# Performance work log

Hardware: AMD Instinct MI355X
Metric: run time of the kernel (lower is better)

Reference implementation:

```python
import jax, jax.numpy as jnp
import numpy as np

N_LAYER, N_HEAD, N_EMBD, VOCAB, T_CTX, MAXT, B = 6, 8, 128, 18, 30, 2719, 64


def _ln(x, g, b, eps=1e-5):
    m = x.mean(-1, keepdims=True)
    v = ((x - m) ** 2).mean(-1, keepdims=True)
    return (x - m) * jax.lax.rsqrt(v + eps) * g + b


def setup_inputs() -> dict:
    key = jax.random.key(0)
    ks = iter(jax.random.split(key, 64))
    nrm = lambda shape: jax.random.normal(next(ks), shape, jnp.float32) * 0.02
    E, L4 = N_EMBD, 4 * N_EMBD
    inp = dict(
        states=jax.random.normal(next(ks), (B, T_CTX, 4, 84, 84), jnp.float32),
        actions=jax.random.randint(next(ks), (B, T_CTX, 1), 0, VOCAB),
        rtgs=jax.random.normal(next(ks), (B, T_CTX, 1), jnp.float32),
        timesteps=jax.random.randint(next(ks), (B, 1, 1), 0, MAXT),
        conv_w=nrm((E, 4, 84, 84)),
        class_tok=nrm((1, 1, E)),
        in_proj_w=nrm((3 * E, E)), in_proj_b=jnp.zeros(3 * E),
        out_w=nrm((E, E)), out_b=jnp.zeros(E),
        iln1_g=jnp.ones(E), iln1_b=jnp.zeros(E),
        iln2_g=jnp.ones(E), iln2_b=jnp.zeros(E),
        ffn_w1=nrm((E, E)), ffn_b1=jnp.zeros(E),
        ffn_w2=nrm((E, E)), ffn_b2=jnp.zeros(E),
        ret_w=nrm((E, 1)), ret_b=jnp.zeros(E),
        act_table=nrm((VOCAB, E)),
        pos_emb=nrm((1, 3 * T_CTX + 1, E)),
        global_pos_emb=nrm((1, MAXT + 1, E)),
        ln1_g=jnp.ones((N_LAYER, E)), ln1_b=jnp.zeros((N_LAYER, E)),
        Wq=nrm((N_LAYER, E, E)), bq=jnp.zeros((N_LAYER, E)),
        Wk=nrm((N_LAYER, E, E)), bk=jnp.zeros((N_LAYER, E)),
        Wv=nrm((N_LAYER, E, E)), bv=jnp.zeros((N_LAYER, E)),
        Wo=nrm((N_LAYER, E, E)), bo=jnp.zeros((N_LAYER, E)),
        ln2_g=jnp.ones((N_LAYER, E)), ln2_b=jnp.zeros((N_LAYER, E)),
        W1=nrm((N_LAYER, L4, E)), b1=jnp.zeros((N_LAYER, L4)),
        W2=nrm((N_LAYER, E, L4)), b2=jnp.zeros((N_LAYER, E)),
        lnf_g=jnp.ones(E), lnf_b=jnp.zeros(E),
        head_w=nrm((VOCAB, E)),
    )
    return inp


def _forward(states, actions, rtgs, timesteps, conv_w, class_tok, in_proj_w, in_proj_b,
             out_w, out_b, iln1_g, iln1_b, iln2_g, iln2_b, ffn_w1, ffn_b1, ffn_w2, ffn_b2,
             ret_w, ret_b, act_table, pos_emb, global_pos_emb,
             ln1_g, ln1_b, Wq, bq, Wk, bk, Wv, bv, Wo, bo, ln2_g, ln2_b,
             W1, b1, W2, b2, lnf_g, lnf_b, head_w):
    Bsz, T = states.shape[:2]
    E = conv_w.shape[0]
    H, hd = N_HEAD, E // N_HEAD
    # --- inner TIT: patch embed (kernel 84 = frame size -> single patch = one big dot) ---
    obs = states.reshape(Bsz * T, *states.shape[2:])                      # (BT,4,84,84)
    patch = jnp.einsum('bchw,echw->be', obs, conv_w)[:, None, :]          # (BT,1,E)
    x = jnp.concatenate([jnp.broadcast_to(class_tok, (Bsz * T, 1, E)), patch], axis=1)  # (BT,2,E)
    h = _ln(x, iln1_g, iln1_b)
    q, k, v = jnp.split(h @ in_proj_w.T + in_proj_b, 3, axis=-1)
    att = jax.nn.softmax(jnp.einsum('bqe,bke->bqk', q, k) / jnp.sqrt(jnp.float32(E)), axis=-1)
    x = x + jnp.einsum('bqk,bke->bqe', att, v) @ out_w.T + out_b
    h2 = _ln(x, iln2_g, iln2_b)
    x = x + jax.nn.relu(h2 @ ffn_w1.T + ffn_b1) @ ffn_w2.T + ffn_b2
    state_emb = x[:, 0, :].reshape(Bsz, T, E)                             # class token
    # --- token interleave (targets=None path -> length 3T-1, last T-1 actions) ---
    rtg_emb = jnp.tanh(rtgs @ ret_w.T + ret_b)                            # (B,T,E)
    act_emb = jnp.tanh(act_table[actions[..., 0]])                        # (B,T,E)
    Lt = 3 * T - 1
    tok = jnp.zeros((Bsz, Lt, E), states.dtype)
    tok = tok.at[:, 0::3].set(rtg_emb).at[:, 1::3].set(state_emb).at[:, 2::3].set(act_emb[:, 1:])
    pos = global_pos_emb[0][timesteps[:, 0, 0]][:, None, :] + pos_emb[:, :Lt, :]
    x = tok + pos
    # --- outer causal GPT blocks ---
    mask = jnp.tril(jnp.ones((Lt, Lt), bool))
    for i in range(N_LAYER):
        hh = _ln(x, ln1_g[i], ln1_b[i])
        proj = lambda w, b: (hh @ w.T + b).reshape(Bsz, Lt, H, hd).transpose(0, 2, 1, 3)
        q, k, v = proj(Wq[i], bq[i]), proj(Wk[i], bk[i]), proj(Wv[i], bv[i])
        att = jnp.einsum('bhqd,bhkd->bhqk', q, k) / jnp.sqrt(jnp.float32(hd))
        att = jax.nn.softmax(jnp.where(mask, att, -jnp.inf), axis=-1)
        y = jnp.einsum('bhqk,bhkd->bhqd', att, v).transpose(0, 2, 1, 3).reshape(Bsz, Lt, E)
        x = x + y @ Wo[i].T + bo[i]
        hh2 = _ln(x, ln2_g[i], ln2_b[i])
        x = x + jax.nn.gelu(hh2 @ W1[i].T + b1[i], approximate=False) @ W2[i].T + b2[i]
    logits = _ln(x, lnf_g, lnf_b) @ head_w.T
    return logits[:, 1::3, :]                                             # (B,T,vocab) state-position logits


def reference(states, actions, rtgs, timesteps, conv_w, class_tok, in_proj_w, in_proj_b,
              out_w, out_b, iln1_g, iln1_b, iln2_g, iln2_b, ffn_w1, ffn_b1, ffn_w2, ffn_b2,
              ret_w, ret_b, act_table, pos_emb, global_pos_emb,
              ln1_g, ln1_b, Wq, bq, Wk, bk, Wv, bv, Wo, bo, ln2_g, ln2_b,
              W1, b1, W2, b2, lnf_g, lnf_b, head_w):
    return _forward(states, actions, rtgs, timesteps, conv_w, class_tok, in_proj_w, in_proj_b,
                    out_w, out_b, iln1_g, iln1_b, iln2_g, iln2_b, ffn_w1, ffn_b1, ffn_w2, ffn_b2,
                    ret_w, ret_b, act_table, pos_emb, global_pos_emb,
                    ln1_g, ln1_b, Wq, bq, Wk, bk, Wv, bv, Wo, bo, ln2_g, ln2_b,
                    W1, b1, W2, b2, lnf_g, lnf_b, head_w)
```

## Files before the change

kernel.cpp:

```cpp
#include <hip/hip_runtime.h>

#define NB   64
#define NT   30
#define NBT  1920
#define EE   128
#define KP   28224
#define LTK  89
#define NS   5696
#define NLY  6
#define NV   18
#define NZ   21

typedef unsigned short ushort_t;
using bf16x8 = __attribute__((ext_vector_type(8))) short;
using us8    = __attribute__((ext_vector_type(8))) unsigned short;
using f32x4  = __attribute__((ext_vector_type(4))) float;
using f32x16 = __attribute__((ext_vector_type(16))) float;

__device__ inline ushort_t f2bf(float f){
  union { float f; unsigned u; } v; v.f = f;
  unsigned r = v.u + 0x7FFFu + ((v.u >> 16) & 1u);
  return (ushort_t)(r >> 16);
}

__global__ __launch_bounds__(256) void wcvt(
  const float* conv, const float* Wq, const float* Wk, const float* Wv,
  const float* Wo, const float* W1, const float* W2,
  const float* in_w, const float* out_w, const float* f1w, const float* f2w,
  const float* bq, const float* bk, const float* bv,
  ushort_t* dc, ushort_t* dqkv, ushort_t* dout, ushort_t* d1, ushort_t* d2,
  ushort_t* dinw, ushort_t* doutw, ushort_t* df1, ushort_t* df2, float* bqkv)
{
  if (blockIdx.x >= 4776){
    int idx = (blockIdx.x-4776)*256 + threadIdx.x;
    if (idx < NLY*128){ int l=idx>>7, j=idx&127;
      bqkv[l*384+j]=bq[idx]; bqkv[l*384+128+j]=bk[idx]; bqkv[l*384+256+j]=bv[idx]; }
    return;
  }
  long i = 4l*((long)blockIdx.x*256 + threadIdx.x);
  if (i >= 3612672l && i < 3907584l){
    long o = i - 3612672l;
    int  seg = (int)(o / 98304l);
    long off2 = o - (long)seg*98304l;
    long layer = off2 >> 14, rem = off2 & 16383l;
    const float* s = (seg==0) ? Wq : (seg==1) ? Wk : Wv;
    float4 f = *reinterpret_cast<const float4*>(s+off2);
    long dst = layer*49152l + (long)seg*16384l + rem;
    dqkv[dst]=f2bf(f.x); dqkv[dst+1]=f2bf(f.y); dqkv[dst+2]=f2bf(f.z); dqkv[dst+3]=f2bf(f.w);
    return;
  }
  const float* s; ushort_t* d; long off;
  if      (i < 3612672l){ s=conv;  d=dc;    off=i; }
  else if (i < 4005888l){ s=Wo;    d=dout;  off=i-3907584l; }
  else if (i < 4399104l){ s=W1;    d=d1;    off=i-4005888l; }
  else if (i < 4792320l){ s=W2;    d=d2;    off=i-4399104l; }
  else if (i < 4841472l){ s=in_w;  d=dinw;  off=i-4792320l; }
  else if (i < 4857856l){ s=out_w; d=doutw; off=i-4841472l; }
  else if (i < 4874240l){ s=f1w;   d=df1;   off=i-4857856l; }
  else                  { s=f2w;   d=df2;   off=i-4874240l; }
  float4 f = *reinterpret_cast<const float4*>(s+off);
  d[off]=f2bf(f.x); d[off+1]=f2bf(f.y); d[off+2]=f2bf(f.z); d[off+3]=f2bf(f.w);
}

__global__ __launch_bounds__(256) void patch_gemm(
  const float* __restrict__ A, const ushort_t* __restrict__ Wb, float* __restrict__ C)
{
  __shared__ __align__(16) ushort_t As[2][64*64];
  __shared__ __align__(16) ushort_t Ws[2][128*64];
  const int tid = threadIdx.x, lane = tid & 63, wid = tid >> 6;
  const int m0 = blockIdx.x * 64;
  const int kbase = blockIdx.z * 1344;
  float* Cz = C + (size_t)blockIdx.z * NBT * EE;
  const int ra = tid>>2, ca = (tid&3)*16, swa = (ra&7)<<3;
  const int rw = tid>>1, cw = (tid&1)*32, sww = (rw&7)<<3;
  const float*    Ab = A  + (size_t)(m0+ra)*KP + kbase + ca;
  const ushort_t* Wp = Wb + (size_t)rw*KP  + kbase + cw;
  f32x4 acc[8];
  #pragma unroll
  for (int j=0;j<8;j++) acc[j] = (f32x4){0.f,0.f,0.f,0.f};

  auto loadT = [&](float4 (&fa)[4], us8 (&wr)[4], int kt){
    #pragma unroll
    for (int q=0;q<4;q++){
      fa[q] = *reinterpret_cast<const float4*>(Ab + kt*64 + 4*q);
      wr[q] = *reinterpret_cast<const us8*>(Wp + kt*64 + 8*q);
    }
  };
  auto commitT = [&](int buf, const float4 (&fa)[4], const us8 (&wr)[4]){
    us8 o0, o1;
    o0[0]=f2bf(fa[0].x); o0[1]=f2bf(fa[0].y); o0[2]=f2bf(fa[0].z); o0[3]=f2bf(fa[0].w);
    o0[4]=f2bf(fa[1].x); o0[5]=f2bf(fa[1].y); o0[6]=f2bf(fa[1].z); o0[7]=f2bf(fa[1].w);
    o1[0]=f2bf(fa[2].x); o1[1]=f2bf(fa[2].y); o1[2]=f2bf(fa[2].z); o1[3]=f2bf(fa[2].w);
    o1[4]=f2bf(fa[3].x); o1[5]=f2bf(fa[3].y); o1[6]=f2bf(fa[3].z); o1[7]=f2bf(fa[3].w);
    *reinterpret_cast<us8*>(&As[buf][ra*64 + ( ca    ^ swa)]) = o0;
    *reinterpret_cast<us8*>(&As[buf][ra*64 + ((ca+8) ^ swa)]) = o1;
    #pragma unroll
    for (int q=0;q<4;q++)
      *reinterpret_cast<us8*>(&Ws[buf][rw*64 + ((cw+8*q) ^ sww)]) = wr[q];
  };
  auto computeT = [&](int buf){
    #pragma unroll
    for (int ks=0; ks<2; ++ks){
      int arow = wid*16 + (lane&15);
      int kb = ks*32 + (lane>>4)*8;
      bf16x8 a = *reinterpret_cast<const bf16x8*>(&As[buf][arow*64 + (kb ^ ((arow&7)<<3))]);
      #pragma unroll
      for (int nt=0; nt<8; ++nt){
        int nn = nt*16 + (lane&15);
        bf16x8 b = *reinterpret_cast<const bf16x8*>(&Ws[buf][nn*64 + (kb ^ ((nn&7)<<3))]);
        acc[nt] = __builtin_amdgcn_mfma_f32_16x16x32_bf16(a, b, acc[nt], 0,0,0);
      }
    }
  };

  float4 faA[4], faB[4]; us8 wrA[4], wrB[4];
  loadT(faA, wrA, 0);
  loadT(faB, wrB, 1);
  for (int kp = 0; kp < 11; ++kp){
    int kt0 = 2*kp;
    commitT(0, faA, wrA);
    if (kt0 + 2 < 21) loadT(faA, wrA, kt0 + 2);
    __syncthreads();
    computeT(0);
    int kt1 = kt0 + 1;
    if (kt1 < 21){
      commitT(1, faB, wrB);
      if (kt1 + 2 < 21) loadT(faB, wrB, kt1 + 2);
      __syncthreads();
      computeT(1);
    }
  }
  #pragma unroll
  for (int nt=0; nt<8; ++nt)
    #pragma unroll
    for (int rr=0;rr<4;rr++){
      int row = m0 + wid*16 + (lane>>4)*4 + rr;
      int col = nt*16 + (lane&15);
      Cz[row*EE + col] = acc[nt][rr];
    }
}

__global__ __launch_bounds__(256, 1) void inner_tit(
  const float* __restrict__ part, const float* __restrict__ ctok,
  const ushort_t* __restrict__ inw, const float* __restrict__ in_b,
  const ushort_t* __restrict__ outw, const float* __restrict__ out_b,
  const float* __restrict__ g1, const float* __restrict__ b1_,
  const float* __restrict__ g2, const float* __restrict__ b2_,
  const ushort_t* __restrict__ f1wb, const float* __restrict__ fb1,
  const ushort_t* __restrict__ f2wb, const float* __restrict__ fb2,
  const float* __restrict__ rtgs, const int* __restrict__ actions,
  const int* __restrict__ tsteps, const float* __restrict__ ret_w,
  const float* __restrict__ ret_b, const float* __restrict__ act_tab,
  const float* __restrict__ pos_emb, const float* __restrict__ gpos,
  const float* __restrict__ ln1g0, const float* __restrict__ ln1b0,
  float* __restrict__ x, ushort_t* __restrict__ xln)
{
  __shared__ __align__(16) ushort_t wbuf[384*128];
  __shared__ float xs[16*128];
  __shared__ __align__(16) ushort_t hb[16*128];
  __shared__ __align__(16) ushort_t hf[16*128];
  __shared__ float qkv[16*384];
  __shared__ float ssm[32];
  const int tid = threadIdx.x, lane = tid & 63, wid = tid >> 6;
  const int bt0 = blockIdx.x * 8;

  auto stageWB = [&](const ushort_t* src, int R, int rowoff){
    for (int c = tid; c < R*16; c += 256){
      int rr = c >> 4, cc = (c & 15) * 8;
      *reinterpret_cast<us8*>(&wbuf[(rowoff+rr)*128 + (cc ^ ((rr&7)<<3))]) =
        *reinterpret_cast<const us8*>(src + (size_t)rr*128 + cc);
    }
  };
  auto lnrow = [&](const float* gam, const float* bet, ushort_t* dst){
    int r = tid >> 4, e0 = (tid & 15) * 8;
    float v[8];
    #pragma unroll
    for (int j=0;j<8;j++) v[j] = xs[r*128 + e0 + j];
    float s = 0;
    #pragma unroll
    for (int j=0;j<8;j++) s += v[j];
    s += __shfl_xor(s,1); s += __shfl_xor(s,2); s += __shfl_xor(s,4); s += __shfl_xor(s,8);
    float mean = s * (1.0f/128.0f);
    float vs = 0;
    #pragma unroll
    for (int j=0;j<8;j++){ float d = v[j]-mean; vs += d*d; }
    vs += __shfl_xor(vs,1); vs += __shfl_xor(vs,2); vs += __shfl_xor(vs,4); vs += __shfl_xor(vs,8);
    float rstd = rsqrtf(vs*(1.0f/128.0f) + 1e-5f);
    us8 o;
    #pragma unroll
    for (int j=0;j<8;j++) o[j] = f2bf((v[j]-mean)*rstd*gam[e0+j] + bet[e0+j]);
    *reinterpret_cast<us8*>(&dst[r*128 + (e0 ^ ((r&7)<<3))]) = o;
  };

  { int r = tid >> 4, e0 = (tid & 15) * 8;
    float v[8];
    if ((r & 1) == 0){
      #pragma unroll
      for (int j=0;j<8;j++) v[j] = ctok[e0+j];
    } else {
      #pragma unroll
      for (int j=0;j<8;j++) v[j] = 0.f;
      int bt = bt0 + (r>>1);
      for (int z=0; z<NZ; ++z){
        const float* p = part + (size_t)z*NBT*EE + (size_t)bt*128 + e0;
        float4 f0 = *reinterpret_cast<const float4*>(p);
        float4 f1 = *reinterpret_cast<const float4*>(p+4);
        v[0]+=f0.x; v[1]+=f0.y; v[2]+=f0.z; v[3]+=f0.w;
        v[4]+=f1.x; v[5]+=f1.y; v[6]+=f1.z; v[7]+=f1.w;
      }
    }
    #pragma unroll
    for (int j=0;j<8;j++) xs[r*128 + e0 + j] = v[j];
  }
  stageWB(inw, 384, 0);
  __syncthreads();

  lnrow(g1, b1_, hb);
  __syncthreads();

  { int al = lane & 15, kq = (lane>>4)*8;
    #pragma unroll
    for (int j=0;j<6;++j){
      int nt = wid*6 + j;
      f32x4 acc = (f32x4){0.f,0.f,0.f,0.f};
      int nrow = nt*16 + al, nsw = (nrow&7)<<3;
      #pragma unroll
      for (int ks=0; ks<4; ++ks){
        int kb = ks*32 + kq;
        bf16x8 a = *reinterpret_cast<const bf16x8*>(&hb[al*128 + (kb ^ ((al&7)<<3))]);
        bf16x8 b = *reinterpret_cast<const bf16x8*>(&wbuf[nrow*128 + (kb ^ nsw)]);
        acc = __builtin_amdgcn_mfma_f32_16x16x32_bf16(a, b, acc, 0,0,0);
      }
      float bia = in_b[nt*16 + al];
      #pragma unroll
      for (int rr=0; rr<4; ++rr){
        int row = (lane>>4)*4 + rr;
        qkv[row*384 + nt*16 + al] = acc[rr] + bia;
      }
    }
  }
  __syncthreads();

  { int d = tid >> 3, j = tid & 7;
    int i = d >> 2, p = d & 3;
    const float* qp = &qkv[(2*i + (p>>1))*384 + j*16];
    const float* kp = &qkv[(2*i + (p&1))*384 + 128 + j*16];
    float s = 0;
    #pragma unroll
    for (int e=0;e<16;e++) s += qp[e]*kp[e];
    s += __shfl_xor(s,1); s += __shfl_xor(s,2); s += __shfl_xor(s,4);
    if (j == 0) ssm[d] = s;
  }
  stageWB(outw, 128, 0);
  stageWB(f1wb, 128, 128);
  stageWB(f2wb, 128, 256);
  __syncthreads();

  { int r = tid >> 4, e0 = (tid & 15)*8;
    int i = r >> 1, t = r & 1;
    const float sc = 0.08838834764831845f;
    float s0 = ssm[i*4 + t*2]*sc, s1 = ssm[i*4 + t*2 + 1]*sc;
    float m = fmaxf(s0,s1), p0 = __expf(s0-m), p1 = __expf(s1-m);
    float iv = 1.0f/(p0+p1); p0 *= iv; p1 *= iv;
    const float* v0 = &qkv[(2*i)*384 + 256 + e0];
    const float* v1 = &qkv[(2*i+1)*384 + 256 + e0];
    us8 o;
    #pragma unroll
    for (int j=0;j<8;j++) o[j] = f2bf(p0*v0[j] + p1*v1[j]);
    *reinterpret_cast<us8*>(&hb[r*128 + (e0 ^ ((r&7)<<3))]) = o;
  }
  __syncthreads();

  { int al = lane & 15, kq = (lane>>4)*8;
    #pragma unroll
    for (int j=0;j<2;++j){
      int nt = wid*2 + j;
      f32x4 acc = (f32x4){0.f,0.f,0.f,0.f};
      int nrow = nt*16 + al, nsw = (nrow&7)<<3;
      #pragma unroll
      for (int ks=0; ks<4; ++ks){
        int kb = ks*32 + kq;
        bf16x8 a = *reinterpret_cast<const bf16x8*>(&hb[al*128 + (kb ^ ((al&7)<<3))]);
        bf16x8 b = *reinterpret_cast<const bf16x8*>(&wbuf[nrow*128 + (kb ^ nsw)]);
        acc = __builtin_amdgcn_mfma_f32_16x16x32_bf16(a, b, acc, 0,0,0);
      }
      float bia = out_b[nt*16 + al];
      #pragma unroll
      for (int rr=0; rr<4; ++rr){
        int row = (lane>>4)*4 + rr;
        xs[row*128 + nt*16 + al] += acc[rr] + bia;
      }
    }
  }
  __syncthreads();

  lnrow(g2, b2_, hb);
  __syncthreads();

  { int al = lane & 15, kq = (lane>>4)*8;
    #pragma unroll
    for (int j=0;j<2;++j){
      int nt = wid*2 + j;
      f32x4 acc = (f32x4){0.f,0.f,0.f,0.f};
      int nrow = nt*16 + al, nsw = (nrow&7)<<3;
      #pragma unroll
      for (int ks=0; ks<4; ++ks){
        int kb = ks*32 + kq;
        bf16x8 a = *reinterpret_cast<const bf16x8*>(&hb[al*128 + (kb ^ ((al&7)<<3))]);
        bf16x8 b = *reinterpret_cast<const bf16x8*>(&wbuf[(128+nrow)*128 + (kb ^ nsw)]);
        acc = __builtin_amdgcn_mfma_f32_16x16x32_bf16(a, b, acc, 0,0,0);
      }
      float bia = fb1[nt*16 + al];
      #pragma unroll
      for (int rr=0; rr<4; ++rr){
        int row = (lane>>4)*4 + rr;
        hf[row*128 + ((nt*16+al) ^ ((row&7)<<3))] = f2bf(fmaxf(acc[rr] + bia, 0.f));
      }
    }
  }
  __syncthreads();

  { int al = lane & 15, kq = (lane>>4)*8;
    #pragma unroll
    for (int j=0;j<2;++j){
      int nt = wid*2 + j;
      f32x4 acc = (f32x4){0.f,0.f,0.f,0.f};
      int nrow = nt*16 + al, nsw = (nrow&7)<<3;
      #pragma unroll
      for (int ks=0; ks<4; ++ks){
        int kb = ks*32 + kq;
        bf16x8 a = *reinterpret_cast<const bf16x8*>(&hf[al*128 + (kb ^ ((al&7)<<3))]);
        bf16x8 b = *reinterpret_cast<const bf16x8*>(&wbuf[(256+nrow)*128 + (kb ^ nsw)]);
        acc = __builtin_amdgcn_mfma_f32_16x16x32_bf16(a, b, acc, 0,0,0);
      }
      float bia = fb2[nt*16 + al];
      #pragma unroll
      for (int rr=0; rr<4; ++rr){
        int row = (lane>>4)*4 + rr;
        xs[row*128 + nt*16 + al] += acc[rr] + bia;
      }
    }
  }
  __syncthreads();

  { int q = tid >> 3, j = tid & 7;
    if (q < 24){
      int i = q / 3, kind = q - 3*i;
      int btg = bt0 + i, b = btg / NT, t = btg - b*NT;
      bool valid = !(kind == 2 && t == 0);
      if (valid){
        int prow = (kind==0) ? 3*t : (kind==1) ? 3*t+1 : 3*t-1;
        size_t xrow = ((size_t)b*LTK + prow)*128;
        int ts = tsteps[b];
        int e0 = j*16;
        float v[16];
        if (kind == 1){
          #pragma unroll
          for (int e=0;e<16;e++) v[e] = xs[(2*i)*128 + e0 + e];
        } else if (kind == 0){
          float rv = rtgs[b*NT+t];
          #pragma unroll
          for (int e=0;e<16;e++) v[e] = tanhf(rv*ret_w[e0+e] + ret_b[e0+e]);
        } else {
          int a = actions[b*NT+t];
          #pragma unroll
          for (int e=0;e<16;e++) v[e] = tanhf(act_tab[a*128 + e0 + e]);
        }
        #pragma unroll
        for (int e=0;e<16;e++)
          v[e] += gpos[(size_t)ts*128 + e0 + e] + pos_emb[prow*128 + e0 + e];
        #pragma unroll
        for (int e=0;e<16;e++) x[xrow + e0 + e] = v[e];
        float s = 0;
        #pragma unroll
        for (int e=0;e<16;e++) s += v[e];
        s += __shfl_xor(s,1); s += __shfl_xor(s,2); s += __shfl_xor(s,4);
        float mean = s * (1.0f/128.0f);
        float vs = 0;
        #pragma unroll
        for (int e=0;e<16;e++){ float d = v[e]-mean; vs += d*d; }
        vs += __shfl_xor(vs,1); vs += __shfl_xor(vs,2); vs += __shfl_xor(vs,4);
        float rstd = rsqrtf(vs*(1.0f/128.0f) + 1e-5f);
        #pragma unroll
        for (int e=0;e<16;e++)
          xln[xrow + e0 + e] = f2bf((v[e]-mean)*rstd*ln1g0[e0+e] + ln1b0[e0+e]);
      }
    }
  }
}

__global__ __launch_bounds__(256, 2) void attn_fused(
  const ushort_t* __restrict__ xln, const ushort_t* __restrict__ Wqkv,
  const float* __restrict__ bqkv, ushort_t* __restrict__ y)
{
  __shared__ __align__(16) char sm[69504];
  ushort_t* ab  = (ushort_t*)sm;
  ushort_t* wb  = (ushort_t*)(sm + 24576);
  float*    S   = (float*)sm;
  ushort_t* qa  = (ushort_t*)(sm + 37248);
  ushort_t* ka  = (ushort_t*)(sm + 41472);
  ushort_t* vta = (ushort_t*)(sm + 45696);
  ushort_t* pb  = (ushort_t*)(sm + 49152);
  float*    inv = (float*)(sm + 69120);

  const int b = blockIdx.x >> 3, h = blockIdx.x & 7;
  const int tid = threadIdx.x, lane = tid & 63, wid = tid >> 6;

  for (int idx = tid; idx < 1536; idx += 256){
    int row = idx >> 4, c0 = (idx & 15) * 8;
    us8 v;
    if (row < LTK) v = *reinterpret_cast<const us8*>(xln + ((size_t)(b*LTK+row))*128 + c0);
    else           v = (us8){0,0,0,0,0,0,0,0};
    *reinterpret_cast<us8*>(&ab[row*128 + (c0 ^ ((row&7)<<3))]) = v;
  }
  for (int idx = tid; idx < 384; idx += 256){
    int rr = idx >> 3, c = (idx & 7) * 16;
    int seg = rr >> 4, n = rr & 15;
    const ushort_t* src = Wqkv + (size_t)(seg*128 + h*16 + n)*128 + c;
    int sw = (rr&7)<<3;
    *reinterpret_cast<us8*>(&wb[rr*128 + ( c    ^ sw)]) = *reinterpret_cast<const us8*>(src);
    *reinterpret_cast<us8*>(&wb[rr*128 + ((c+8) ^ sw)]) = *reinterpret_cast<const us8*>(src+8);
  }
  __syncthreads();

  for (int idx = wid; idx < 18; idx += 4){
    int rt = idx / 3, nt = idx - 3*(idx/3);
    f32x4 acc = (f32x4){0.f,0.f,0.f,0.f};
    int arow = rt*16 + (lane&15), asw = (arow&7)<<3;
    int nrow = nt*16 + (lane&15), nsw = (nrow&7)<<3;
    #pragma unroll
    for (int ks=0; ks<4; ++ks){
      int kb = ks*32 + (lane>>4)*8;
      bf16x8 a = *reinterpret_cast<const bf16x8*>(&ab[arow*128 + (kb ^ asw)]);
      bf16x8 bf = *reinterpret_cast<const bf16x8*>(&wb[nrow*128 + (kb ^ nsw)]);
      acc = __builtin_amdgcn_mfma_f32_16x16x32_bf16(a, bf, acc, 0,0,0);
    }
    int d = lane & 15;
    float bia = bqkv[nt*128 + h*16 + d];
    #pragma unroll
    for (int rr=0; rr<4; ++rr){
      int rg = rt*16 + (lane>>4)*4 + rr;
      ushort_t hv = f2bf(acc[rr] + bia);
      if      (nt == 0) qa[rg*22 + d] = hv;
      else if (nt == 1) ka[rg*22 + d] = hv;
      else              vta[d*108 + rg] = hv;
    }
  }
  __syncthreads();

  {
    static const int TR[6] = {0,1,1,2,2,2};
    static const int TC[6] = {0,0,1,0,1,2};
    for (int idx = wid; idx < 6; idx += 4){
      int R = TR[idx], C = TC[idx];
      int arow = R*32 + (lane&31), brow = C*32 + (lane&31);
      int ke = (lane>>5)*8;
      bf16x8 a  = *reinterpret_cast<const bf16x8*>(&qa[arow*22 + ke]);
      bf16x8 bf = *reinterpret_cast<const bf16x8*>(&ka[brow*22 + ke]);
      f32x16 sc = {};
      sc = __builtin_amdgcn_mfma_f32_32x32x16_bf16(a, bf, sc, 0,0,0);
      #pragma unroll
      for (int r=0; r<16; ++r){
        int rin = (r&3) + 8*(r>>2) + 4*(lane>>5);
        S[(R*32+rin)*97 + C*32 + (lane&31)] = sc[r]*0.25f;
      }
    }
  }
  __syncthreads();

  if (tid < 192){
    int t = tid >> 1, half = tid & 1;
    int u0 = half*48;
    float mx = -1e30f;
    if (t < LTK){
      for (int u=u0; u<u0+48; ++u) if (u<=t) mx = fmaxf(mx, S[t*97+u]);
    }
    mx = fmaxf(mx, __shfl_xor(mx,1));
    float smv = 0;
    if (t < LTK){
      for (int u=u0; u<u0+48; ++u){
        float p = 0;
        if (u<=t){ p = __expf(S[t*97+u]-mx); smv += p; }
        pb[t*104+u] = f2bf(p);
      }
    } else {
      for (int u=u0; u<u0+48; ++u) pb[t*104+u] = 0;
    }
    smv += __shfl_xor(smv,1);
    if (half==0) inv[t] = (t<LTK) ? 1.0f/smv : 0.0f;
  }
  __syncthreads();

  for (int rt = wid; rt < 6; rt += 4){
    int arow = rt*16 + (lane&15);
    f32x4 acc = (f32x4){0.f,0.f,0.f,0.f};
    #pragma unroll
    for (int ks=0; ks<3; ++ks){
      int kb = ks*32 + (lane>>4)*8;
      bf16x8 a  = *reinterpret_cast<const bf16x8*>(&pb[arow*104 + kb]);
      bf16x8 bf = *reinterpret_cast<const bf16x8*>(&vta[(lane&15)*108 + kb]);
      acc = __builtin_amdgcn_mfma_f32_16x16x32_bf16(a, bf, acc, 0,0,0);
    }
    #pragma unroll
    for (int rr=0; rr<4; ++rr){
      int rg = rt*16 + (lane>>4)*4 + rr;
      if (rg < LTK)
        y[(size_t)(b*LTK+rg)*128 + h*16 + (lane&15)] = f2bf(acc[rr]*inv[rg]);
    }
  }
}

template<bool HEAD>
__global__ __launch_bounds__(256, 2) void ffn_fused(
  const ushort_t* __restrict__ yg, const ushort_t* __restrict__ Wo,
  const float* __restrict__ bo, const float* __restrict__ g2,
  const float* __restrict__ b2g, const ushort_t* __restrict__ W1,
  const float* __restrict__ b1v, const ushort_t* __restrict__ W2,
  const float* __restrict__ b2v, float* __restrict__ x,
  const float* __restrict__ lnng, const float* __restrict__ lnnb,
  ushort_t* __restrict__ xlnout,
  const float* __restrict__ lnfg, const float* __restrict__ lnfb,
  const float* __restrict__ hw, float* __restrict__ out)
{
  __shared__ __align__(16) char sm[66304];
  ushort_t* wdb = (ushort_t*)sm;
  float*    xr  = (float*)(sm + 32768);
  ushort_t* h2  = (ushort_t*)(sm + 49664);
  ushort_t* f1  = (ushort_t*)(sm + 57856);
  const int tid = threadIdx.x, lane = tid & 63, wid = tid >> 6;
  const int m0 = blockIdx.x * 32;
  const int rr = tid >> 2, qq = tid & 3, swr = (rr&7)<<3;

  auto srcp = [&](int s)->const ushort_t* {
    if (s == 0) return Wo + (size_t)rr*128 + qq*32;
    if (s == 1) return Wo + (size_t)(64+rr)*128 + qq*32;
    int c = (s-2)>>2, r = (s-2)&3;
    if (r == 0) return W1 + (size_t)(c*128+rr)*128 + qq*32;
    if (r == 1) return W1 + (size_t)(c*128+64+rr)*128 + qq*32;
    if (r == 2) return W2 + (size_t)rr*512 + c*128 + qq*32;
    return W2 + (size_t)(64+rr)*512 + c*128 + qq*32;
  };
  auto issue = [&](us8 (&r)[4], int s){
    const ushort_t* p = srcp(s);
    #pragma unroll
    for (int g=0; g<4; ++g) r[g] = *reinterpret_cast<const us8*>(p + 8*g);
  };
  auto commit = [&](int buf, const us8 (&r)[4]){
    ushort_t* d = wdb + buf*8192 + rr*128;
    #pragma unroll
    for (int g=0; g<4; ++g)
      *reinterpret_cast<us8*>(&d[(qq*32+8*g) ^ swr]) = r[g];
  };
  auto gemmT = [&](const ushort_t* abuf, int buf, f32x4* accp){
    int nrow = wid*16 + (lane&15), nsw = (nrow&7)<<3;
    const ushort_t* wbp = wdb + buf*8192;
    #pragma unroll
    for (int rt=0; rt<2; ++rt){
      int arow = rt*16 + (lane&15), asw = (arow&7)<<3;
      #pragma unroll
      for (int ks=0; ks<4; ++ks){
        int kb = ks*32 + (lane>>4)*8;
        bf16x8 a  = *reinterpret_cast<const bf16x8*>(&abuf[arow*128 + (kb ^ asw)]);
        bf16x8 bb = *reinterpret_cast<const bf16x8*>(&wdb[buf*8192 + nrow*128 + (kb ^ nsw)]);
        accp[rt] = __builtin_amdgcn_mfma_f32_16x16x32_bf16(a, bb, accp[rt], 0,0,0);
      }
    }
    (void)wbp;
  };

  f32x4 accA[2][2], acc2[2][2];
  #pragma unroll
  for (int s_=0;s_<2;++s_){
    accA[s_][0]=(f32x4){0,0,0,0}; accA[s_][1]=(f32x4){0,0,0,0};
    acc2[s_][0]=(f32x4){0,0,0,0}; acc2[s_][1]=(f32x4){0,0,0,0};
  }

  auto computeStage = [&](int k, int buf){
    if (k == 0){
      gemmT(f1, buf, accA[0]);
    } else if (k == 1){
      gemmT(f1, buf, accA[1]);
      #pragma unroll
      for (int s_=0; s_<2; ++s_){
        int col = s_*64 + wid*16 + (lane&15);
        float bia = bo[col];
        #pragma unroll
        for (int rt=0; rt<2; ++rt)
          #pragma unroll
          for (int r4=0; r4<4; ++r4){
            int row = rt*16 + (lane>>4)*4 + r4;
            xr[row*132 + col] = accA[s_][rt][r4] + bia + x[(size_t)(m0+row)*128 + col];
          }
      }
      __syncthreads();
      { int r8 = tid>>3, q8 = tid&7;
        float xv[16];
        #pragma unroll
        for (int i=0;i<16;i++) xv[i] = xr[r8*132 + q8*16 + i];
        float s = 0;
        #pragma unroll
        for (int i=0;i<16;i++) s += xv[i];
        s += __shfl_xor(s,1); s += __shfl_xor(s,2); s += __shfl_xor(s,4);
        float mean = s * (1.0f/128.0f);
        float vs = 0;
        #pragma unroll
        for (int i=0;i<16;i++){ float d = xv[i]-mean; vs += d*d; }
        vs += __shfl_xor(vs,1); vs += __shfl_xor(vs,2); vs += __shfl_xor(vs,4);
        float rstd = rsqrtf(vs*(1.0f/128.0f) + 1e-5f);
        int sw = (r8&7)<<3;
        #pragma unroll
        for (int g=0; g<2; ++g){
          us8 o;
          #pragma unroll
          for (int jj=0;jj<8;jj++){
            int c = q8*16 + g*8 + jj;
            o[jj] = f2bf((xv[g*8+jj]-mean)*rstd*g2[c] + b2g[c]);
          }
          *reinterpret_cast<us8*>(&h2[r8*128 + ((q8*16+g*8) ^ sw)]) = o;
        }
      }
    } else {
      int r = (k-2)&3, c = (k-2)>>2;
      if (r < 2){
        f32x4 ac[2] = {(f32x4){0,0,0,0},(f32x4){0,0,0,0}};
        gemmT(h2, buf, ac);
        int cl = r*64 + wid*16 + (lane&15);
        float bia = b1v[c*128 + cl];
        #pragma unroll
        for (int rt=0; rt<2; ++rt)
          #pragma unroll
          for (int r4=0; r4<4; ++r4){
            int row = rt*16 + (lane>>4)*4 + r4;
            float v = ac[rt][r4] + bia;
            v = 0.5f*v*(1.0f + erff(v*0.70710678118654752f));
            f1[row*128 + (cl ^ ((row&7)<<3))] = f2bf(v);
          }
      } else if (r == 2){
        gemmT(f1, buf, acc2[0]);
      } else {
        gemmT(f1, buf, acc2[1]);
      }
    }
  };

  { int r8 = tid>>3, q8 = tid&7, sw = (r8&7)<<3;
    const ushort_t* src = yg + (size_t)(m0+r8)*128 + q8*16;
    *reinterpret_cast<us8*>(&f1[r8*128 + ((q8*16)   ^ sw)]) = *reinterpret_cast<const us8*>(src);
    *reinterpret_cast<us8*>(&f1[r8*128 + ((q8*16+8) ^ sw)]) = *reinterpret_cast<const us8*>(src+8);
  }
  us8 rA[4], rB[4];
  issue(rA, 0); issue(rB, 1);

  for (int kp = 0; kp < 9; ++kp){
    int k0 = 2*kp, k1 = 2*kp + 1;
    commit(0, rA);
    if (k0 + 2 < 18) issue(rA, k0 + 2);
    __syncthreads();
    computeStage(k0, 0);
    commit(1, rB);
    if (k1 + 2 < 18) issue(rB, k1 + 2);
    __syncthreads();
    computeStage(k1, 1);
  }

  #pragma unroll
  for (int s_=0; s_<2; ++s_){
    int col = s_*64 + wid*16 + (lane&15);
    float bia = b2v[col];
    #pragma unroll
    for (int rt=0; rt<2; ++rt)
      #pragma unroll
      for (int r4=0; r4<4; ++r4){
        int row = rt*16 + (lane>>4)*4 + r4;
        float v = acc2[s_][rt][r4] + bia + xr[row*132 + col];
        xr[row*132 + col] = v;
        if constexpr (!HEAD) x[(size_t)(m0+row)*128 + col] = v;
      }
  }
  __syncthreads();
  if constexpr (!HEAD){
    int r8 = tid>>3, q8 = tid&7;
    float xv[16];
    #pragma unroll
    for (int i=0;i<16;i++) xv[i] = xr[r8*132 + q8*16 + i];
    float s = 0;
    #pragma unroll
    for (int i=0;i<16;i++) s += xv[i];
    s += __shfl_xor(s,1); s += __shfl_xor(s,2); s += __shfl_xor(s,4);
    float mean = s * (1.0f/128.0f);
    float vs = 0;
    #pragma unroll
    for (int i=0;i<16;i++){ float d = xv[i]-mean; vs += d*d; }
    vs += __shfl_xor(vs,1); vs += __shfl_xor(vs,2); vs += __shfl_xor(vs,4);
    float rstd = rsqrtf(vs*(1.0f/128.0f) + 1e-5f);
    #pragma unroll
    for (int g=0; g<2; ++g){
      us8 o;
      #pragma unroll
      for (int jj=0;jj<8;jj++){
        int c = q8*16 + g*8 + jj;
        o[jj] = f2bf((xv[g*8+jj]-mean)*rstd*lnng[c] + lnnb[c]);
      }
      *reinterpret_cast<us8*>(xlnout + (size_t)(m0+r8)*128 + q8*16 + g*8) = o;
    }
  } else {
    for (int r = wid; r < 32; r += 4){
      int s = m0 + r, bb2 = s / LTK, p = s - bb2*LTK;
      if (p % 3 != 1) continue;
      int t = p / 3;
      float v1 = xr[r*132 + lane];
      float v2 = xr[r*132 + 64 + lane];
      float sum = v1 + v2;
      sum += __shfl_xor(sum,1); sum += __shfl_xor(sum,2); sum += __shfl_xor(sum,4);
      sum += __shfl_xor(sum,8); sum += __shfl_xor(sum,16); sum += __shfl_xor(sum,32);
      float mean = sum*(1.0f/128.0f);
      float d1 = v1-mean, d2 = v2-mean;
      float var = d1*d1 + d2*d2;
      var += __shfl_xor(var,1); var += __shfl_xor(var,2); var += __shfl_xor(var,4);
      var += __shfl_xor(var,8); var += __shfl_xor(var,16); var += __shfl_xor(var,32);
      float rstd = rsqrtf(var*(1.0f/128.0f) + 1e-5f);
      float h1 = d1*rstd*lnfg[lane]    + lnfb[lane];
      float h2v= d2*rstd*lnfg[lane+64] + lnfb[lane+64];
      #pragma unroll
      for (int o=0; o<NV; ++o){
        float sdot = h1*hw[o*128+lane] + h2v*hw[o*128+lane+64];
        sdot += __shfl_xor(sdot,1); sdot += __shfl_xor(sdot,2); sdot += __shfl_xor(sdot,4);
        sdot += __shfl_xor(sdot,8); sdot += __shfl_xor(sdot,16); sdot += __shfl_xor(sdot,32);
        if (lane == 0) out[(size_t)(bb2*NT+t)*NV + o] = sdot;
      }
    }
  }
}

extern "C" void kernel_launch(void* const* d_in, const int* in_sizes, int n_in,
                              void* d_out, int out_size, void* d_ws, size_t ws_size,
                              hipStream_t stream)
{
  const float* states  = (const float*)d_in[0];
  const int*   actions = (const int*)  d_in[1];
  const float* rtgs    = (const float*)d_in[2];
  const int*   tsteps  = (const int*)  d_in[3];
  const float* conv_w  = (const float*)d_in[4];
  const float* ctok    = (const float*)d_in[5];
  const float* in_w    = (const float*)d_in[6];
  const float* in_b    = (const float*)d_in[7];
  const float* out_w   = (const float*)d_in[8];
  const float* out_b   = (const float*)d_in[9];
  const float* i1g     = (const float*)d_in[10];
  const float* i1b     = (const float*)d_in[11];
  const float* i2g     = (const float*)d_in[12];
  const float* i2b     = (const float*)d_in[13];
  const float* fw1     = (const float*)d_in[14];
  const float* fb1     = (const float*)d_in[15];
  const float* fw2     = (const float*)d_in[16];
  const float* fb2     = (const float*)d_in[17];
  const float* ret_w   = (const float*)d_in[18];
  const float* ret_b   = (const float*)d_in[19];
  const float* act_tab = (const float*)d_in[20];
  const float* pos_emb = (const float*)d_in[21];
  const float* gpos    = (const float*)d_in[22];
  const float* ln1g    = (const float*)d_in[23];
  const float* ln1b    = (const float*)d_in[24];
  const float* Wq      = (const float*)d_in[25];
  const float* bq      = (const float*)d_in[26];
  const float* Wk      = (const float*)d_in[27];
  const float* bk      = (const float*)d_in[28];
  const float* Wv      = (const float*)d_in[29];
  const float* bv      = (const float*)d_in[30];
  const float* Wo      = (const float*)d_in[31];
  const float* bo      = (const float*)d_in[32];
  const float* ln2g    = (const float*)d_in[33];
  const float* ln2b    = (const float*)d_in[34];
  const float* W1      = (const float*)d_in[35];
  const float* b1      = (const float*)d_in[36];
  const float* W2      = (const float*)d_in[37];
  const float* b2      = (const float*)d_in[38];
  const float* lnfg    = (const float*)d_in[39];
  const float* lnfb    = (const float*)d_in[40];
  const float* head_w  = (const float*)d_in[41];

  char* w = (char*)d_ws;
  size_t off = 0;
  auto alloc = [&](size_t bytes)->char* {
    char* p = w + off; off += (bytes + 255) & ~(size_t)255; return p;
  };
  float*    part  = (float*)   alloc((size_t)NZ*NBT*EE*4);
  float*    x     = (float*)   alloc((size_t)NS*EE*4);
  ushort_t* xlnA  = (ushort_t*)alloc((size_t)NS*EE*2);
  ushort_t* xlnB  = (ushort_t*)alloc((size_t)NS*EE*2);
  ushort_t* yb    = (ushort_t*)alloc((size_t)NS*EE*2);
  ushort_t* cwb   = (ushort_t*)alloc((size_t)EE*KP*2);
  ushort_t* Wqkvb = (ushort_t*)alloc((size_t)NLY*384*128*2);
  ushort_t* Wob   = (ushort_t*)alloc((size_t)NLY*128*128*2);
  ushort_t* W1b   = (ushort_t*)alloc((size_t)NLY*512*128*2);
  ushort_t* W2b   = (ushort_t*)alloc((size_t)NLY*128*512*2);
  ushort_t* inwb  = (ushort_t*)alloc((size_t)384*128*2);
  ushort_t* outwb = (ushort_t*)alloc((size_t)128*128*2);
  ushort_t* f1wb  = (ushort_t*)alloc((size_t)128*128*2);
  ushort_t* f2wb  = (ushort_t*)alloc((size_t)128*128*2);
  float*    bqkv  = (float*)   alloc(NLY*384*4);
  (void)in_sizes; (void)n_in; (void)out_size; (void)ws_size;

  wcvt<<<4779,256,0,stream>>>(conv_w,Wq,Wk,Wv,Wo,W1,W2,
                              in_w,out_w,fw1,fw2, bq,bk,bv,
                              cwb,Wqkvb,Wob,W1b,W2b,
                              inwb,outwb,f1wb,f2wb, bqkv);
  patch_gemm<<<dim3(30,1,NZ),256,0,stream>>>(states, cwb, part);
  inner_tit<<<240,256,0,stream>>>(part, ctok, inwb, in_b, outwb, out_b,
                                  i1g,i1b,i2g,i2b, f1wb,fb1, f2wb,fb2,
                                  rtgs, actions, tsteps, ret_w, ret_b, act_tab,
                                  pos_emb, gpos, ln1g, ln1b, x, xlnA);
  for (int i=0;i<NLY;i++){
    ushort_t* xin  = (i & 1) ? xlnB : xlnA;
    ushort_t* xout = (i & 1) ? xlnA : xlnB;
    attn_fused<<<512,256,0,stream>>>(
      xin, Wqkvb+(size_t)i*49152, bqkv+(size_t)i*384, yb);
    if (i < NLY-1)
      ffn_fused<false><<<178,256,0,stream>>>(
        yb, Wob+(size_t)i*16384, bo+i*128, ln2g+i*128, ln2b+i*128,
        W1b+(size_t)i*65536, b1+i*512, W2b+(size_t)i*65536, b2+i*128, x,
        ln1g+(i+1)*128, ln1b+(i+1)*128, xout,
        nullptr, nullptr, nullptr, nullptr);
    else
      ffn_fused<true><<<178,256,0,stream>>>(
        yb, Wob+(size_t)i*16384, bo+i*128, ln2g+i*128, ln2b+i*128,
        W1b+(size_t)i*65536, b1+i*512, W2b+(size_t)i*65536, b2+i*128, x,
        nullptr, nullptr, nullptr,
        lnfg, lnfb, head_w, (float*)d_out);
  }
}
```

Baseline: 315.8 us.

## Shrink inner_tit LDS footprint to allow two blocks per CU

```diff
diff --git a/kernel.cpp b/kernel.cpp
--- a/kernel.cpp
+++ b/kernel.cpp
@@ -21,6 +21,9 @@
   union { float f; unsigned u; } v; v.f = f;
   unsigned r = v.u + 0x7FFFu + ((v.u >> 16) & 1u);
   return (ushort_t)(r >> 16);
+}
+__device__ inline float bf2f(ushort_t h){
+  union { unsigned u; float f; } v; v.u = ((unsigned)h) << 16; return v.f;
 }
 
 __global__ __launch_bounds__(256) void wcvt(
@@ -140,7 +143,7 @@
     }
 }
 
-__global__ __launch_bounds__(256, 1) void inner_tit(
+__global__ __launch_bounds__(256, 2) void inner_tit(
   const float* __restrict__ part, const float* __restrict__ ctok,
   const ushort_t* __restrict__ inw, const float* __restrict__ in_b,
   const ushort_t* __restrict__ outw, const float* __restrict__ out_b,
@@ -155,19 +158,19 @@
   const float* __restrict__ ln1g0, const float* __restrict__ ln1b0,
   float* __restrict__ x, ushort_t* __restrict__ xln)
 {
-  __shared__ __align__(16) ushort_t wbuf[384*128];
+  __shared__ __align__(16) ushort_t wbuf[192*128];
   __shared__ float xs[16*128];
   __shared__ __align__(16) ushort_t hb[16*128];
   __shared__ __align__(16) ushort_t hf[16*128];
-  __shared__ float qkv[16*384];
+  __shared__ __align__(16) ushort_t qkvb[16*400];
   __shared__ float ssm[32];
   const int tid = threadIdx.x, lane = tid & 63, wid = tid >> 6;
   const int bt0 = blockIdx.x * 8;
 
-  auto stageWB = [&](const ushort_t* src, int R, int rowoff){
+  auto stageWB = [&](const ushort_t* src, int R){
     for (int c = tid; c < R*16; c += 256){
       int rr = c >> 4, cc = (c & 15) * 8;
-      *reinterpret_cast<us8*>(&wbuf[(rowoff+rr)*128 + (cc ^ ((rr&7)<<3))]) =
+      *reinterpret_cast<us8*>(&wbuf[rr*128 + (cc ^ ((rr&7)<<3))]) =
         *reinterpret_cast<const us8*>(src + (size_t)rr*128 + cc);
     }
   };
@@ -190,6 +193,17 @@
     #pragma unroll
     for (int j=0;j<8;j++) o[j] = f2bf((v[j]-mean)*rstd*gam[e0+j] + bet[e0+j]);
     *reinterpret_cast<us8*>(&dst[r*128 + (e0 ^ ((r&7)<<3))]) = o;
+  };
+  auto qgemm = [&](const ushort_t* abuf, int ntg, int rowoff, f32x4& acc){
+    int al = lane & 15, kq = (lane>>4)*8;
+    int nrow = (ntg*16 + al) - rowoff, nsw = (nrow&7)<<3;
+    #pragma unroll
+    for (int ks=0; ks<4; ++ks){
+      int kb = ks*32 + kq;
+      bf16x8 a = *reinterpret_cast<const bf16x8*>(&abuf[al*128 + (kb ^ ((al&7)<<3))]);
+      bf16x8 b = *reinterpret_cast<const bf16x8*>(&wbuf[nrow*128 + (kb ^ nsw)]);
+      acc = __builtin_amdgcn_mfma_f32_16x16x32_bf16(a, b, acc, 0,0,0);
+    }
   };
 
   { int r = tid >> 4, e0 = (tid & 15) * 8;
@@ -212,30 +226,40 @@
     #pragma unroll
     for (int j=0;j<8;j++) xs[r*128 + e0 + j] = v[j];
   }
-  stageWB(inw, 384, 0);
+  stageWB(inw, 192);
   __syncthreads();
 
   lnrow(g1, b1_, hb);
   __syncthreads();
 
-  { int al = lane & 15, kq = (lane>>4)*8;
-    #pragma unroll
-    for (int j=0;j<6;++j){
-      int nt = wid*6 + j;
+  { int al = lane & 15;
+    #pragma unroll
+    for (int j=0;j<3;++j){
+      int nt = wid*3 + j;
       f32x4 acc = (f32x4){0.f,0.f,0.f,0.f};
-      int nrow = nt*16 + al, nsw = (nrow&7)<<3;
-      #pragma unroll
-      for (int ks=0; ks<4; ++ks){
-        int kb = ks*32 + kq;
-        bf16x8 a = *reinterpret_cast<const bf16x8*>(&hb[al*128 + (kb ^ ((al&7)<<3))]);
-        bf16x8 b = *reinterpret_cast<const bf16x8*>(&wbuf[nrow*128 + (kb ^ nsw)]);
-        acc = __builtin_amdgcn_mfma_f32_16x16x32_bf16(a, b, acc, 0,0,0);
-      }
+      qgemm(hb, nt, 0, acc);
       float bia = in_b[nt*16 + al];
       #pragma unroll
       for (int rr=0; rr<4; ++rr){
         int row = (lane>>4)*4 + rr;
-        qkv[row*384 + nt*16 + al] = acc[rr] + bia;
+        qkvb[row*400 + nt*16 + al] = f2bf(acc[rr] + bia);
+      }
+    }
+  }
+  __syncthreads();
+  stageWB(inw + (size_t)192*128, 192);
+  __syncthreads();
+  { int al = lane & 15;
+    #pragma unroll
+    for (int j=0;j<3;++j){
+      int nt = 12 + wid*3 + j;
+      f32x4 acc = (f32x4){0.f,0.f,0.f,0.f};
+      qgemm(hb, nt, 192, acc);
+      float bia = in_b[nt*16 + al];
+      #pragma unroll
+      for (int rr=0; rr<4; ++rr){
+        int row = (lane>>4)*4 + rr;
+        qkvb[row*400 + nt*16 + al] = f2bf(acc[rr] + bia);
       }
     }
   }
@@ -243,17 +267,15 @@
 
   { int d = tid >> 3, j = tid & 7;
     int i = d >> 2, p = d & 3;
-    const float* qp = &qkv[(2*i + (p>>1))*384 + j*16];
-    const float* kp = &qkv[(2*i + (p&1))*384 + 128 + j*16];
+    const ushort_t* qp = &qkvb[(2*i + (p>>1))*400 + j*16];
+    const ushort_t* kp = &qkvb[(2*i + (p&1))*400 + 128 + j*16];
     float s = 0;
     #pragma unroll
-    for (int e=0;e<16;e++) s += qp[e]*kp[e];
+    for (int e=0;e<16;e++) s += bf2f(qp[e])*bf2f(kp[e]);
     s += __shfl_xor(s,1); s += __shfl_xor(s,2); s += __shfl_xor(s,4);
     if (j == 0) ssm[d] = s;
   }
-  stageWB(outw, 128, 0);
-  stageWB(f1wb, 128, 128);
-  stageWB(f2wb, 128, 256);
+  stageWB(outw, 128);
   __syncthreads();
 
   { int r = tid >> 4, e0 = (tid & 15)*8;
@@ -262,28 +284,21 @@
     float s0 = ssm[i*4 + t*2]*sc, s1 = ssm[i*4 + t*2 + 1]*sc;
     float m = fmaxf(s0,s1), p0 = __expf(s0-m), p1 = __expf(s1-m);
     float iv = 1.0f/(p0+p1); p0 *= iv; p1 *= iv;
-    const float* v0 = &qkv[(2*i)*384 + 256 + e0];
-    const float* v1 = &qkv[(2*i+1)*384 + 256 + e0];
+    const ushort_t* v0 = &qkvb[(2*i)*400 + 256 + e0];
+    const ushort_t* v1 = &qkvb[(2*i+1)*400 + 256 + e0];
     us8 o;
     #pragma unroll
-    for (int j=0;j<8;j++) o[j] = f2bf(p0*v0[j] + p1*v1[j]);
+    for (int j=0;j<8;j++) o[j] = f2bf(p0*bf2f(v0[j]) + p1*bf2f(v1[j]));
     *reinterpret_cast<us8*>(&hb[r*128 + (e0 ^ ((r&7)<<3))]) = o;
   }
   __syncthreads();
 
-  { int al = lane & 15, kq = (lane>>4)*8;
+  { int al = lane & 15;
     #pragma unroll
     for (int j=0;j<2;++j){
       int nt = wid*2 + j;
       f32x4 acc = (f32x4){0.f,0.f,0.f,0.f};
-      int nrow = nt*16 + al, nsw = (nrow&7)<<3;
-      #pragma unroll
-      for (int ks=0; ks<4; ++ks){
-        int kb = ks*32 + kq;
-        bf16x8 a = *reinterpret_cast<const bf16x8*>(&hb[al*128 + (kb ^ ((al&7)<<3))]);
-        bf16x8 b = *reinterpret_cast<const bf16x8*>(&wbuf[nrow*128 + (kb ^ nsw)]);
-        acc = __builtin_amdgcn_mfma_f32_16x16x32_bf16(a, b, acc, 0,0,0);
-      }
+      qgemm(hb, nt, 0, acc);
       float bia = out_b[nt*16 + al];
       #pragma unroll
       for (int rr=0; rr<4; ++rr){
@@ -295,21 +310,15 @@
   __syncthreads();
 
   lnrow(g2, b2_, hb);
-  __syncthreads();
-
-  { int al = lane & 15, kq = (lane>>4)*8;
+  stageWB(f1wb, 128);
+  __syncthreads();
+
+  { int al = lane & 15;
     #pragma unroll
     for (int j=0;j<2;++j){
       int nt = wid*2 + j;
       f32x4 acc = (f32x4){0.f,0.f,0.f,0.f};
-      int nrow = nt*16 + al, nsw = (nrow&7)<<3;
-      #pragma unroll
-      for (int ks=0; ks<4; ++ks){
-        int kb = ks*32 + kq;
-        bf16x8 a = *reinterpret_cast<const bf16x8*>(&hb[al*128 + (kb ^ ((al&7)<<3))]);
-        bf16x8 b = *reinterpret_cast<const bf16x8*>(&wbuf[(128+nrow)*128 + (kb ^ nsw)]);
-        acc = __builtin_amdgcn_mfma_f32_16x16x32_bf16(a, b, acc, 0,0,0);
-      }
+      qgemm(hb, nt, 0, acc);
       float bia = fb1[nt*16 + al];
       #pragma unroll
       for (int rr=0; rr<4; ++rr){
@@ -320,19 +329,14 @@
   }
   __syncthreads();
 
-  { int al = lane & 15, kq = (lane>>4)*8;
+  stageWB(f2wb, 128);
+  __syncthreads();
+  { int al = lane & 15;
     #pragma unroll
     for (int j=0;j<2;++j){
       int nt = wid*2 + j;
       f32x4 acc = (f32x4){0.f,0.f,0.f,0.f};
-      int nrow = nt*16 + al, nsw = (nrow&7)<<3;
-      #pragma unroll
-      for (int ks=0; ks<4; ++ks){
-        int kb = ks*32 + kq;
-        bf16x8 a = *reinterpret_cast<const bf16x8*>(&hf[al*128 + (kb ^ ((al&7)<<3))]);
-        bf16x8 b = *reinterpret_cast<const bf16x8*>(&wbuf[(256+nrow)*128 + (kb ^ nsw)]);
-        acc = __builtin_amdgcn_mfma_f32_16x16x32_bf16(a, b, acc, 0,0,0);
-      }
+      qgemm(hf, nt, 0, acc);
       float bia = fb2[nt*16 + al];
       #pragma unroll
       for (int rr=0; rr<4; ++rr){
@@ -553,7 +557,6 @@
   };
   auto gemmT = [&](const ushort_t* abuf, int buf, f32x4* accp){
     int nrow = wid*16 + (lane&15), nsw = (nrow&7)<<3;
-    const ushort_t* wbp = wdb + buf*8192;
     #pragma unroll
     for (int rt=0; rt<2; ++rt){
       int arow = rt*16 + (lane&15), asw = (arow&7)<<3;
@@ -565,7 +568,6 @@
         accp[rt] = __builtin_amdgcn_mfma_f32_16x16x32_bf16(a, bb, accp[rt], 0,0,0);
       }
     }
-    (void)wbp;
   };
 
   f32x4 accA[2][2], acc2[2][2];
```

After: 317.0 us. No clear change (+0.4%).
